# Kernel optimization log

Measured on AMD Instinct MI355X. Metric: run time of the kernel, lower is better.

Reference implementation:

```python
import jax, jax.numpy as jnp
import numpy as np

N_WIRES = 10
N_OPS = 30
C64 = jnp.complex64

# Frozen random circuit (stand-in for tq.RandomLayer(n_ops=30)): deterministic op list.
_rng = np.random.default_rng(42)
OPS = []
for _ in range(N_OPS):
    k = int(_rng.integers(0, 4))
    if k == 3:
        w = _rng.choice(N_WIRES, size=2, replace=False)
        OPS.append(('cnot', int(w[0]), int(w[1])))
    else:
        OPS.append((('rx', 'ry', 'rz')[k], int(_rng.integers(0, N_WIRES)), -1))


def _rx_mat(t):
    c = jnp.cos(t / 2).astype(C64)
    s = jnp.sin(t / 2).astype(C64)
    return jnp.stack([jnp.stack([c, -1j * s]), jnp.stack([-1j * s, c])])


def _ry_mat(t):
    c = jnp.cos(t / 2).astype(C64)
    s = jnp.sin(t / 2).astype(C64)
    return jnp.stack([jnp.stack([c, -s]), jnp.stack([s, c])])


def _rz_mat(t):
    tc = t.astype(C64)
    z = jnp.zeros((), C64)
    return jnp.stack([jnp.stack([jnp.exp(-1j * tc / 2), z]), jnp.stack([z, jnp.exp(1j * tc / 2)])])

_GATE = {'rx': _rx_mat, 'ry': _ry_mat, 'rz': _rz_mat}


def _apply_1q(state, U, w):
    # state: [bsz] + [2]*N_WIRES ; apply 2x2 U on qubit axis w
    s = jnp.moveaxis(state, 1 + w, -1)
    s = jnp.einsum('ij,...j->...i', U, s)
    return jnp.moveaxis(s, -1, 1 + w)


def _apply_cnot(state, c, t):
    s = jnp.moveaxis(state, (1 + c, 1 + t), (-2, -1))
    s = jnp.stack([s[..., 0, :], s[..., 1, ::-1]], axis=-2)  # flip target when control=1
    return jnp.moveaxis(s, (-2, -1), (1 + c, 1 + t))


def _quantum_head(x, rand_params, rx_theta, ry_theta, head_w, head_b):
    bsz = x.shape[0]
    # GeneralEncoder '10xRy': RY(x[:,w])|0> per wire -> product state built directly
    state = jnp.ones((bsz, 1), C64)
    for w in range(N_WIRES):
        vec = jnp.stack([jnp.cos(x[:, w] / 2), jnp.sin(x[:, w] / 2)], axis=-1).astype(C64)
        state = (state[:, :, None] * vec[:, None, :]).reshape(bsz, -1)
    state = state.reshape((bsz,) + (2,) * N_WIRES)
    # RandomLayer (frozen 30-op circuit, one angle per op)
    for i, (kind, a, b) in enumerate(OPS):
        if kind == 'cnot':
            state = _apply_cnot(state, a, b)
        else:
            state = _apply_1q(state, _GATE[kind](rand_params[i]), a)
    # shared trainable RX then RY applied to every wire (single shared param each)
    Urx = _rx_mat(rx_theta[0])
    Ury = _ry_mat(ry_theta[0])
    for w in range(N_WIRES):
        state = _apply_1q(state, Urx, w)
        state = _apply_1q(state, Ury, w)
    # MeasureAll(PauliZ): <Z_w> = P(bit_w=0) - P(bit_w=1)
    probs = jnp.abs(state) ** 2  # float32, [bsz] + [2]*n
    feats = []
    for w in range(N_WIRES):
        axes = tuple(1 + q for q in range(N_WIRES) if q != w)
        p = probs.sum(axis=axes)  # [bsz, 2]
        feats.append(p[:, 0] - p[:, 1])
    feats = jnp.stack(feats, axis=-1)  # [bsz, n_wires]
    return feats @ head_w + head_b[0]


def _mlp(x, w0, b0, w1, b1, w2, b2, w3, b3):
    # faithful to ClassicalMLP: Linear chain with NO activations
    h = x @ w0.T + b0
    h = h @ w1.T + b1
    h = h @ w2.T + b2
    return (h @ w3.T + b3)[:, 0]


def setup_inputs() -> dict:
    key = jax.random.key(0)
    ks = jax.random.split(key, 14)
    BSZ = 8192
    return {
        'state_batch': jax.random.normal(ks[0], (BSZ, N_WIRES), jnp.float32),
        'rand_params': jax.random.normal(ks[1], (N_OPS,), jnp.float32),
        'rx_theta': jax.random.normal(ks[2], (1,), jnp.float32),
        'ry_theta': jax.random.normal(ks[3], (1,), jnp.float32),
        'head_w': jax.random.normal(ks[4], (N_WIRES,), jnp.float32) * 0.3,
        'head_b': jax.random.normal(ks[5], (1,), jnp.float32) * 0.1,
        'w0': jax.random.normal(ks[6], (64, N_WIRES), jnp.float32) * 0.3,
        'b0': jax.random.normal(ks[7], (64,), jnp.float32) * 0.1,
        'w1': jax.random.normal(ks[8], (32, 64), jnp.float32) * 0.12,
        'b1': jax.random.normal(ks[9], (32,), jnp.float32) * 0.1,
        'w2': jax.random.normal(ks[10], (16, 32), jnp.float32) * 0.17,
        'b2': jax.random.normal(ks[11], (16,), jnp.float32) * 0.1,
        'w3': jax.random.normal(ks[12], (1, 16), jnp.float32) * 0.25,
        'b3': jax.random.normal(ks[13], (1,), jnp.float32) * 0.1,
    }


def reference(state_batch, rand_params, rx_theta, ry_theta, head_w, head_b, w0, b0, w1, b1, w2, b2, w3, b3):
    q = _quantum_head(state_batch, rand_params, rx_theta, ry_theta, head_w, head_b)
    c = _mlp(state_batch, w0, b0, w1, b1, w2, b2, w3, b3)
    return q + c
```

## Files before the change

kernel.cpp:

```cpp
#include <hip/hip_runtime.h>
#include <cstdint>

#define NW 10
#define NOPS 30

namespace {

typedef unsigned __int128 u128;

struct CRng { u128 state; u128 inc; bool has32; uint32_t cached; };

constexpr u128 PCG_MUL = (((u128)0x2360ED051FC65DA4ULL) << 64) | (u128)0x4385DF649FCCF645ULL;

constexpr void cr_step(CRng &r) { r.state = r.state * PCG_MUL + r.inc; }

constexpr uint64_t cr_out(u128 st) {
  uint64_t hi = (uint64_t)(st >> 64);
  uint64_t lo = (uint64_t)st;
  unsigned rot = (unsigned)(st >> 122) & 63u;
  uint64_t v = hi ^ lo;
  return (v >> rot) | (v << ((64u - rot) & 63u));
}

constexpr uint64_t cr_next64(CRng &r) { cr_step(r); return cr_out(r.state); }

constexpr uint32_t cr_next32(CRng &r) {
  if (r.has32) { r.has32 = false; return r.cached; }
  uint64_t v = cr_next64(r);
  r.has32 = true; r.cached = (uint32_t)(v >> 32);
  return (uint32_t)v;
}

constexpr CRng cr_seed(uint32_t ent) {
  uint32_t pool[4] = {0u, 0u, 0u, 0u};
  uint32_t hc = 0x43b0d7e5u;
  for (int i = 0; i < 4; i++) {
    uint32_t v = (i == 0) ? ent : 0u;
    v ^= hc; hc *= 0x931e8875u; v *= hc; v ^= v >> 16;
    pool[i] = v;
  }
  for (int s = 0; s < 4; s++)
    for (int d = 0; d < 4; d++)
      if (s != d) {
        uint32_t v = pool[s];
        v ^= hc; hc *= 0x931e8875u; v *= hc; v ^= v >> 16;
        uint32_t res = 0xca01f9ddu * pool[d] - 0x4973f715u * v;
        res ^= res >> 16;
        pool[d] = res;
      }
  uint32_t hb = 0x8b51f9ddu;
  uint64_t s64[4] = {0ull, 0ull, 0ull, 0ull};
  for (int i = 0; i < 8; i++) {
    uint32_t d = pool[i & 3];
    d ^= hb; hb *= 0x58f38dedu; d *= hb; d ^= d >> 16;
    if (i & 1) s64[i >> 1] |= ((uint64_t)d << 32); else s64[i >> 1] = (uint64_t)d;
  }
  CRng r{};
  u128 initstate = (((u128)s64[0]) << 64) | (u128)s64[1];
  u128 initseq   = (((u128)s64[2]) << 64) | (u128)s64[3];
  r.state = 0; r.inc = (initseq << 1) | (u128)1;
  cr_step(r);
  r.state += initstate;
  cr_step(r);
  r.has32 = false; r.cached = 0u;
  return r;
}

constexpr uint32_t cr_lemire32(CRng &r, uint32_t rng) {
  uint32_t rng_excl = rng + 1u;
  uint64_t m = (uint64_t)cr_next32(r) * (uint64_t)rng_excl;
  uint32_t leftover = (uint32_t)m;
  if (leftover < rng_excl) {
    uint32_t threshold = (uint32_t)(0xFFFFFFFFu - rng) % rng_excl;
    while (leftover < threshold) {
      m = (uint64_t)cr_next32(r) * (uint64_t)rng_excl;
      leftover = (uint32_t)m;
    }
  }
  return (uint32_t)(m >> 32);
}

constexpr bool canary_pcg42() {
  CRng r = cr_seed(42u);
  double a = (double)(cr_next64(r) >> 11) * (1.0 / 9007199254740992.0);
  double b = (double)(cr_next64(r) >> 11) * (1.0 / 9007199254740992.0);
  double c = (double)(cr_next64(r) >> 11) * (1.0 / 9007199254740992.0);
  bool ok = (a > 0.77395603) && (a < 0.77395607);
  ok = ok && (b > 0.43887842) && (b < 0.43887846);
  ok = ok && (c > 0.85859790) && (c < 0.85859794);
  return ok;
}
static_assert(canary_pcg42(), "CANARY_PCG_SEED42_RANDOM_MISMATCH");

struct COp { int kind; int a; int b; int slot; };
struct Circ { COp op[NOPS]; };

constexpr Circ build_circuit() {
  Circ c{};
  CRng r = cr_seed(42u);
  for (int i = 0; i < NOPS; i++) {
    int k = (int)cr_lemire32(r, 3u);
    if (k == 3) {
      uint32_t v8 = cr_lemire32(r, 8u);
      uint32_t v9 = cr_lemire32(r, 9u);
      uint32_t i0 = v8;
      uint32_t i1 = (v9 == v8) ? 9u : v9;
      uint32_t j = cr_lemire32(r, 1u);
      if (j == 0u) { uint32_t t = i0; i0 = i1; i1 = t; }
      c.op[i] = COp{3, (int)i0, (int)i1, i};
    } else {
      int w = (int)cr_lemire32(r, 9u);
      c.op[i] = COp{k, w, 0, i};
    }
  }
  return c;
}
constexpr Circ CC = build_circuit();

constexpr int MAXP = 16384;
constexpr int MAXU = 4096;

struct Tables {
  int np, nu, overflow;
  uint32_t pmeta[MAXP]; uint32_t pcm[MAXP]; uint32_t psm[MAXP];
  uint32_t ukey[MAXU];  int ustart[MAXU + 1];
};

constexpr Tables build_tables() {
  Tables T{};
  uint32_t meta[MAXP] = {}; uint32_t cm[MAXP] = {}; uint32_t sm[MAXP] = {};
  int np = 0; int ovf = 0;
  for (int w = 0; w < NW; w++)
    for (int src = 0; src < 3; src++) {
      uint32_t xm = (src != 0) ? (1u << w) : 0u;
      uint32_t zm = (src != 1) ? (1u << w) : 0u;
      meta[np] = xm | (zm << 10) | ((uint32_t)w << 21) | ((uint32_t)src << 25);
      cm[np] = 0u; sm[np] = 0u; np++;
    }
  for (int k = NOPS - 1; k >= 0 && !ovf; k--) {
    const COp op = CC.op[k];
    if (op.kind == 3) {
      const int c = op.a, t = op.b;
      for (int p = 0; p < np; p++) {
        uint32_t m = meta[p];
        uint32_t xm = m & 1023u, zm = (m >> 10) & 1023u;
        uint32_t xc = (xm >> c) & 1u, zc = (zm >> c) & 1u;
        uint32_t xt = (xm >> t) & 1u, zt = (zm >> t) & 1u;
        uint32_t fl = xc & zt & (1u ^ (xt ^ zc));
        xm ^= xc << t;
        zm ^= zt << c;
        m = (m & ~(1023u | (1023u << 10))) | xm | (zm << 10);
        m ^= fl << 20;
        meta[p] = m;
      }
    } else {
      const int q = op.a, ax = op.kind, bit = op.slot;
      const int n0 = np;
      for (int p = 0; p < n0; p++) {
        uint32_t m = meta[p];
        uint32_t x = (m >> q) & 1u;
        uint32_t z = (m >> (10 + q)) & 1u;
        uint32_t viol = (ax == 0) ? z : (ax == 1) ? (x ^ z) : x;
        if (viol) {
          uint32_t nx = 0, nz = 0, fl = 0;
          if (ax == 0)      { if (x) { nx = 0; nz = 1; fl = 1; } else { nx = 1; nz = 1; fl = 0; } }
          else if (ax == 1) { if (x) { nx = 0; nz = 1; fl = 0; } else { nx = 1; nz = 0; fl = 1; } }
          else              { if (z) { nx = 1; nz = 0; fl = 0; } else { nx = 1; nz = 1; fl = 1; } }
          if (np >= MAXP) { ovf = 1; break; }
          uint32_t m2 = m;
          m2 &= ~((1u << q) | (1u << (10 + q)));
          m2 |= (nx << q) | (nz << (10 + q));
          m2 ^= fl << 20;
          meta[np] = m2; cm[np] = cm[p]; sm[np] = sm[p] | (1u << bit);
          np++;
          cm[p] |= 1u << bit;
        }
      }
    }
  }
  if (ovf) { T.overflow = 1; return T; }
  int n2 = 0;
  for (int p = 0; p < np; p++) {
    uint32_t m = meta[p];
    if ((m & 1023u) & ((m >> 10) & 1023u)) continue;
    meta[n2] = m; cm[n2] = cm[p]; sm[n2] = sm[p]; n2++;
  }
  np = n2;
  int idx[MAXP] = {}; int tmp[MAXP] = {};
  for (int i = 0; i < np; i++) idx[i] = i;
  int hist[1025] = {};
  for (int i = 0; i < 1025; i++) hist[i] = 0;
  for (int i = 0; i < np; i++) hist[1 + (meta[idx[i]] & 1023u)]++;
  for (int i = 0; i < 1024; i++) hist[i + 1] += hist[i];
  for (int i = 0; i < np; i++) tmp[hist[meta[idx[i]] & 1023u]++] = idx[i];
  for (int i = 0; i < 1025; i++) hist[i] = 0;
  for (int i = 0; i < np; i++) hist[1 + ((meta[tmp[i]] >> 10) & 1023u)]++;
  for (int i = 0; i < 1024; i++) hist[i + 1] += hist[i];
  for (int i = 0; i < np; i++) idx[hist[(meta[tmp[i]] >> 10) & 1023u]++] = tmp[i];
  int nu = 0; uint32_t prev = 0xFFFFFFFFu;
  for (int i = 0; i < np; i++) {
    int p = idx[i];
    uint32_t key = meta[p] & 0xFFFFFu;
    if (key != prev) {
      if (nu >= MAXU) { T.overflow = 2; return T; }
      T.ukey[nu] = key; T.ustart[nu] = i; prev = key; nu++;
    }
    T.pmeta[i] = meta[p]; T.pcm[i] = cm[p]; T.psm[i] = sm[p];
  }
  T.ustart[nu] = np;
  T.np = np; T.nu = nu; T.overflow = 0;
  return T;
}

constexpr Tables TT = build_tables();
static_assert(TT.overflow == 0, "PAULI_PATH_OVERFLOW_raise_MAXP_or_pivot_to_runtime_tables");
static_assert(TT.nu >= 1 && TT.nu <= MAXU, "PAULI_UNIQUE_COUNT_OUT_OF_RANGE");
constexpr int NU = TT.nu;

}

__device__ const Tables dTT = TT;

__global__ __launch_bounds__(256) void prep_kernel(
    const float* __restrict__ rand_params,
    const float* __restrict__ rx_theta, const float* __restrict__ ry_theta,
    const float* __restrict__ head_w, const float* __restrict__ head_b,
    const float* __restrict__ w0, const float* __restrict__ b0,
    const float* __restrict__ w1, const float* __restrict__ b1,
    const float* __restrict__ w2, const float* __restrict__ b2,
    const float* __restrict__ w3, const float* __restrict__ b3,
    float* __restrict__ ws)
{
  const int tid = threadIdx.x;
  __shared__ float ct[32], st[32], abr[3], hwsh[10];
  __shared__ float r2[32], r1[64];

  if (tid < NOPS) {
    float t = rand_params[tid];
    ct[tid] = cosf(t);
    st[tid] = sinf(t);
  }
  if (tid == 30) {
    float tx = rx_theta[0], ty = ry_theta[0];
    abr[0] = cosf(tx) * cosf(ty);
    abr[1] = -sinf(ty);
    abr[2] = sinf(tx) * cosf(ty);
  }
  if (tid < NW) hwsh[tid] = head_w[tid];
  __syncthreads();

  for (int u = tid; u < NU; u += 256) {
    float acc = 0.f;
    const int i0 = dTT.ustart[u], i1 = dTT.ustart[u + 1];
    for (int i = i0; i < i1; i++) {
      uint32_t m = dTT.pmeta[i];
      float v = hwsh[(m >> 21) & 15u] * abr[(m >> 25) & 3u];
      if (m & (1u << 20)) v = -v;
      uint32_t c = dTT.pcm[i];
      while (c) { int b = __builtin_ctz(c); v *= ct[b]; c &= c - 1u; }
      uint32_t s = dTT.psm[i];
      while (s) { int b = __builtin_ctz(s); v *= st[b]; s &= s - 1u; }
      acc += v;
    }
    ws[u] = acc;
  }

  if (tid < 32) {
    float acc = 0.f;
    for (int k = 0; k < 16; k++) acc += w3[k] * w2[k*32 + tid];
    r2[tid] = acc;
  }
  __syncthreads();
  if (tid < 64) {
    float acc = 0.f;
    for (int k = 0; k < 32; k++) acc += r2[k] * w1[k*64 + tid];
    r1[tid] = acc;
  }
  __syncthreads();
  if (tid < NW) {
    float acc = 0.f;
    for (int k = 0; k < 64; k++) acc += r1[k] * w0[k*NW + tid];
    ws[NU + tid] = acc;
  }
  if (tid == NW) {
    float acc = b3[0] + head_b[0];
    for (int k = 0; k < 16; k++) acc += w3[k] * b2[k];
    for (int k = 0; k < 32; k++) acc += r2[k] * b1[k];
    for (int k = 0; k < 64; k++) acc += r1[k] * b0[k];
    ws[NU + NW] = acc;
  }
}

__global__ __launch_bounds__(256) void qsim_kernel(
    const float* __restrict__ x,
    const float* __restrict__ ws,
    float* __restrict__ out,
    int bsz)
{
  __shared__ float    Csh[NU];
  __shared__ uint32_t Ksh[NU];
  const int tid = threadIdx.x;
  for (int i = tid; i < NU; i += 256) {
    Csh[i] = ws[i];
    Ksh[i] = dTT.ukey[i];
  }
  __syncthreads();

  const int wv = (int)((blockIdx.x * blockDim.x + tid) >> 6);
  const int lane = tid & 63;
  if (wv >= bsz) return;
  const float* xe = x + wv * NW;

  float cz[NW], sx[NW];
#pragma unroll
  for (int w = 0; w < NW; w++) {
    float xv = xe[w];
    cz[w] = __cosf(xv);
    sx[w] = __sinf(xv);
  }

  float acc = 0.f;
  for (int s = lane; s < NU; s += 64) {
    uint32_t k = Ksh[s];
    float v = Csh[s];
#pragma unroll
    for (int w = 0; w < NW; w++) {
      float f = ((k >> w) & 1u) ? sx[w]
              : (((k >> (10 + w)) & 1u) ? cz[w] : 1.0f);
      v *= f;
    }
    acc += v;
  }

#pragma unroll
  for (int m = 1; m < 64; m <<= 1) acc += __shfl_xor(acc, m);

  if (lane == 0) {
    float cc = ws[NU + NW];
#pragma unroll
    for (int w = 0; w < NW; w++) cc += xe[w] * ws[NU + w];
    out[wv] = acc + cc;
  }
}

extern "C" void kernel_launch(void* const* d_in, const int* in_sizes, int n_in,
                              void* d_out, int out_size, void* d_ws, size_t ws_size,
                              hipStream_t stream) {
  const float* x   = (const float*)d_in[0];
  const float* rp  = (const float*)d_in[1];
  const float* rxT = (const float*)d_in[2];
  const float* ryT = (const float*)d_in[3];
  const float* hw  = (const float*)d_in[4];
  const float* hb  = (const float*)d_in[5];
  const float* w0  = (const float*)d_in[6];
  const float* b0  = (const float*)d_in[7];
  const float* w1  = (const float*)d_in[8];
  const float* b1  = (const float*)d_in[9];
  const float* w2  = (const float*)d_in[10];
  const float* b2  = (const float*)d_in[11];
  const float* w3  = (const float*)d_in[12];
  const float* b3  = (const float*)d_in[13];
  const int bsz = in_sizes[0] / NW;

  float* ws = (float*)d_ws;

  hipLaunchKernelGGL(prep_kernel, dim3(1), dim3(256), 0, stream,
                     rp, rxT, ryT, hw, hb, w0, b0, w1, b1, w2, b2, w3, b3, ws);

  const int blocks = (bsz + 3) / 4;
  hipLaunchKernelGGL(qsim_kernel, dim3(blocks), dim3(256), 0, stream,
                     x, ws, (float*)d_out, bsz);
}
```

Measured before the change: 93.59 us.

## Use per-wire-pair lookup tables and packed keys; parallelize prep over blocks

```diff
diff --git a/kernel.cpp b/kernel.cpp
--- a/kernel.cpp
+++ b/kernel.cpp
@@ -124,6 +124,7 @@
   int np, nu, overflow;
   uint32_t pmeta[MAXP]; uint32_t pcm[MAXP]; uint32_t psm[MAXP];
   uint32_t ukey[MAXU];  int ustart[MAXU + 1];
+  uint32_t upk[MAXU];
 };
 
 constexpr Tables build_tables() {
@@ -208,6 +209,15 @@
     T.pmeta[i] = meta[p]; T.pcm[i] = cm[p]; T.psm[i] = sm[p];
   }
   T.ustart[nu] = np;
+  for (int u = 0; u < nu; u++) {
+    uint32_t key = T.ukey[u]; uint32_t pk = 0;
+    for (int p = 0; p < 5; p++) {
+      uint32_t x2 = (key >> (2 * p)) & 3u;
+      uint32_t z2 = (key >> (10 + 2 * p)) & 3u;
+      pk |= ((x2 | (z2 << 2)) << 2) << (6 * p);
+    }
+    T.upk[u] = pk;
+  }
   T.np = np; T.nu = nu; T.overflow = 0;
   return T;
 }
@@ -215,7 +225,8 @@
 constexpr Tables TT = build_tables();
 static_assert(TT.overflow == 0, "PAULI_PATH_OVERFLOW_raise_MAXP_or_pivot_to_runtime_tables");
 static_assert(TT.nu >= 1 && TT.nu <= MAXU, "PAULI_UNIQUE_COUNT_OUT_OF_RANGE");
-constexpr int NU = TT.nu;
+constexpr int NU  = TT.nu;
+constexpr int NUP = (NU + 1) & ~1;
 
 }
 
@@ -249,7 +260,9 @@
   if (tid < NW) hwsh[tid] = head_w[tid];
   __syncthreads();
 
-  for (int u = tid; u < NU; u += 256) {
+  const int u = blockIdx.x * 256 + tid;
+  float2* ws2 = (float2*)ws;
+  if (u < NU) {
     float acc = 0.f;
     const int i0 = dTT.ustart[u], i1 = dTT.ustart[u + 1];
     for (int i = i0; i < i1; i++) {
@@ -262,32 +275,36 @@
       while (s) { int b = __builtin_ctz(s); v *= st[b]; s &= s - 1u; }
       acc += v;
     }
-    ws[u] = acc;
-  }
-
-  if (tid < 32) {
-    float acc = 0.f;
-    for (int k = 0; k < 16; k++) acc += w3[k] * w2[k*32 + tid];
-    r2[tid] = acc;
-  }
-  __syncthreads();
-  if (tid < 64) {
-    float acc = 0.f;
-    for (int k = 0; k < 32; k++) acc += r2[k] * w1[k*64 + tid];
-    r1[tid] = acc;
-  }
-  __syncthreads();
-  if (tid < NW) {
-    float acc = 0.f;
-    for (int k = 0; k < 64; k++) acc += r1[k] * w0[k*NW + tid];
-    ws[NU + tid] = acc;
-  }
-  if (tid == NW) {
-    float acc = b3[0] + head_b[0];
-    for (int k = 0; k < 16; k++) acc += w3[k] * b2[k];
-    for (int k = 0; k < 32; k++) acc += r2[k] * b1[k];
-    for (int k = 0; k < 64; k++) acc += r1[k] * b0[k];
-    ws[NU + NW] = acc;
+    ws2[u] = make_float2(acc, __uint_as_float(dTT.upk[u]));
+  } else if (u < NUP) {
+    ws2[u] = make_float2(0.f, __uint_as_float(0u));
+  }
+
+  if (blockIdx.x == 0) {
+    if (tid < 32) {
+      float acc = 0.f;
+      for (int k = 0; k < 16; k++) acc += w3[k] * w2[k * 32 + tid];
+      r2[tid] = acc;
+    }
+    __syncthreads();
+    if (tid < 64) {
+      float acc = 0.f;
+      for (int k = 0; k < 32; k++) acc += r2[k] * w1[k * 64 + tid];
+      r1[tid] = acc;
+    }
+    __syncthreads();
+    if (tid < NW) {
+      float acc = 0.f;
+      for (int k = 0; k < 64; k++) acc += r1[k] * w0[k * NW + tid];
+      ws[2 * NUP + tid] = acc;
+    }
+    if (tid == NW) {
+      float acc = b3[0] + head_b[0];
+      for (int k = 0; k < 16; k++) acc += w3[k] * b2[k];
+      for (int k = 0; k < 32; k++) acc += r2[k] * b1[k];
+      for (int k = 0; k < 64; k++) acc += r1[k] * b0[k];
+      ws[2 * NUP + NW] = acc;
+    }
   }
 }
 
@@ -297,48 +314,74 @@
     float* __restrict__ out,
     int bsz)
 {
-  __shared__ float    Csh[NU];
-  __shared__ uint32_t Ksh[NU];
+  __shared__ __align__(16) float2 CKsh[NUP];
+  __shared__ float Tbl[4][80];
+  __shared__ float MLPsh[NW + 1];
   const int tid = threadIdx.x;
-  for (int i = tid; i < NU; i += 256) {
-    Csh[i] = ws[i];
-    Ksh[i] = dTT.ukey[i];
-  }
-  __syncthreads();
+  const float2* ws2 = (const float2*)ws;
+  for (int i = tid; i < NUP; i += 256) CKsh[i] = ws2[i];
+  if (tid < NW + 1) MLPsh[tid] = ws[2 * NUP + tid];
 
   const int wv = (int)((blockIdx.x * blockDim.x + tid) >> 6);
   const int lane = tid & 63;
-  if (wv >= bsz) return;
+  float* tbl = Tbl[tid >> 6];
+  const bool live = (wv < bsz);
   const float* xe = x + wv * NW;
 
-  float cz[NW], sx[NW];
-#pragma unroll
-  for (int w = 0; w < NW; w++) {
-    float xv = xe[w];
-    cz[w] = __cosf(xv);
-    sx[w] = __sinf(xv);
-  }
-
-  float acc = 0.f;
-  for (int s = lane; s < NU; s += 64) {
-    uint32_t k = Ksh[s];
-    float v = Csh[s];
-#pragma unroll
-    for (int w = 0; w < NW; w++) {
-      float f = ((k >> w) & 1u) ? sx[w]
-              : (((k >> (10 + w)) & 1u) ? cz[w] : 1.0f);
-      v *= f;
-    }
-    acc += v;
-  }
+  if (live) {
+    {
+      const int e = lane;
+      const int p = e >> 4, code = e & 15;
+      float2 xv = *(const float2*)(xe + 2 * p);
+      float c0 = __cosf(xv.x), s0 = __sinf(xv.x);
+      float c1 = __cosf(xv.y), s1 = __sinf(xv.y);
+      float f0 = (code & 1) ? s0 : ((code & 4) ? c0 : 1.0f);
+      float f1 = (code & 2) ? s1 : ((code & 8) ? c1 : 1.0f);
+      tbl[e] = f0 * f1;
+    }
+    if (lane < 16) {
+      const int e = lane + 64;
+      const int p = e >> 4, code = e & 15;
+      float2 xv = *(const float2*)(xe + 2 * p);
+      float c0 = __cosf(xv.x), s0 = __sinf(xv.x);
+      float c1 = __cosf(xv.y), s1 = __sinf(xv.y);
+      float f0 = (code & 1) ? s0 : ((code & 4) ? c0 : 1.0f);
+      float f1 = (code & 2) ? s1 : ((code & 8) ? c1 : 1.0f);
+      tbl[e] = f0 * f1;
+    }
+  }
+  __syncthreads();
+  if (!live) return;
+
+  const char* tb = (const char*)tbl;
+  float acc0 = 0.f, acc1 = 0.f;
+#pragma unroll 4
+  for (int s = 2 * lane; s < NUP; s += 128) {
+    float4 q = *(const float4*)&CKsh[s];
+    uint32_t ka = __float_as_uint(q.y);
+    uint32_t kb = __float_as_uint(q.w);
+    float a0 = *(const float*)(tb +       ( ka        & 63u));
+    float a1 = *(const float*)(tb +  64 + ((ka >>  6) & 63u));
+    float a2 = *(const float*)(tb + 128 + ((ka >> 12) & 63u));
+    float a3 = *(const float*)(tb + 192 + ((ka >> 18) & 63u));
+    float a4 = *(const float*)(tb + 256 + ((ka >> 24) & 63u));
+    float b0 = *(const float*)(tb +       ( kb        & 63u));
+    float b1 = *(const float*)(tb +  64 + ((kb >>  6) & 63u));
+    float b2 = *(const float*)(tb + 128 + ((kb >> 12) & 63u));
+    float b3 = *(const float*)(tb + 192 + ((kb >> 18) & 63u));
+    float b4 = *(const float*)(tb + 256 + ((kb >> 24) & 63u));
+    acc0 = fmaf(q.x, ((a0 * a1) * (a2 * a3)) * a4, acc0);
+    acc1 = fmaf(q.z, ((b0 * b1) * (b2 * b3)) * b4, acc1);
+  }
+  float acc = acc0 + acc1;
 
 #pragma unroll
   for (int m = 1; m < 64; m <<= 1) acc += __shfl_xor(acc, m);
 
   if (lane == 0) {
-    float cc = ws[NU + NW];
+    float cc = MLPsh[NW];
 #pragma unroll
-    for (int w = 0; w < NW; w++) cc += xe[w] * ws[NU + w];
+    for (int w = 0; w < NW; w++) cc += xe[w] * MLPsh[w];
     out[wv] = acc + cc;
   }
 }
@@ -364,7 +407,8 @@
 
   float* ws = (float*)d_ws;
 
-  hipLaunchKernelGGL(prep_kernel, dim3(1), dim3(256), 0, stream,
+  const int prep_blocks = (NUP + 255) / 256;
+  hipLaunchKernelGGL(prep_kernel, dim3(prep_blocks), dim3(256), 0, stream,
                      rp, rxT, ryT, hw, hb, w0, b0, w1, b1, w2, b2, w3, b3, ws);
 
   const int blocks = (bsz + 3) / 4;
```

New measurement: 94.80 us. No clear change (+1.3%).
